# Kernel optimization log

Hardware: AMD Instinct MI355X
Metric: run time of the kernel (lower is better)

Reference implementation:

```python
import jax, jax.numpy as jnp
import numpy as np

N_NODES = 100000
F_DIM = 128      # graph.num_node_features
TE_DIM = 32      # te_emb_dim
D = F_DIM + TE_DIM  # attention embed_dim = 160
B = 4096         # number of target nodes (batched python loop)
K = 64           # candidates per target
TAU = 1.0
THRESHOLD = 0.2
EPS = 1e-10


def setup_inputs() -> dict:
    key = jax.random.key(0)
    ks = jax.random.split(key, 16)
    inp = {
        "x": jax.random.normal(ks[0], (N_NODES, F_DIM), dtype=jnp.float32),
        "target_node_ids": jax.random.randint(ks[1], (B,), 0, N_NODES),
        "target_node_times": jax.random.randint(ks[2], (B,), 1, 10000),
        "neighbor_ids": jax.random.randint(ks[3], (B, K), 0, N_NODES),
        "edge_time": jax.random.randint(ks[4], (B, K), 0, 10000),
        "edge_weight": jax.random.uniform(ks[5], (B, K), dtype=jnp.float32),
        "gumbel_u": jax.random.uniform(ks[6], (B, K), dtype=jnp.float32),
        # TemporalEncoding params: te(t) = cos(t * w + b)
        "te_w": jax.random.normal(ks[7], (TE_DIM,), dtype=jnp.float32),
        "te_b": jax.random.normal(ks[8], (TE_DIM,), dtype=jnp.float32),
        # MultiheadAttention params (packed qkv like torch)
        "in_proj_w": jax.random.normal(ks[9], (3 * D, D), dtype=jnp.float32) / np.sqrt(D),
        "in_proj_b": jnp.zeros((3 * D,), dtype=jnp.float32),
        "out_w": jax.random.normal(ks[10], (D, D), dtype=jnp.float32) / np.sqrt(D),
        "out_b": jnp.zeros((D,), dtype=jnp.float32),
        # MLP: Linear(D+1 -> 1) + LeakyReLU
        "mlp_w": jax.random.normal(ks[11], (D + 1,), dtype=jnp.float32) / np.sqrt(D + 1),
        "mlp_b": jnp.zeros((1,), dtype=jnp.float32),
    }
    return inp


def reference(x, target_node_ids, target_node_times, neighbor_ids, edge_time,
              edge_weight, gumbel_u, te_w, te_b, in_proj_w, in_proj_b,
              out_w, out_b, mlp_w, mlp_b):
    # --- build target embedding: [B, D]
    t_x = x[target_node_ids]                                          # [B, F]
    t_te = jnp.cos(target_node_times[:, None].astype(jnp.float32) * te_w + te_b)  # [B, TE]
    q_in = jnp.concatenate([t_x, t_te], axis=-1)                      # [B, D]

    # --- candidate embeddings: [B, K, D]
    c_x = x[neighbor_ids]                                             # [B, K, F]
    c_te = jnp.cos(edge_time[..., None].astype(jnp.float32) * te_w + te_b)        # [B, K, TE]
    kv_in = jnp.concatenate([c_x, c_te], axis=-1)                     # [B, K, D]

    # --- single-head MultiheadAttention (eval mode, 1 query per target)
    Wq, Wk, Wv = in_proj_w[:D], in_proj_w[D:2 * D], in_proj_w[2 * D:]
    bq, bk, bv = in_proj_b[:D], in_proj_b[D:2 * D], in_proj_b[2 * D:]
    q = q_in @ Wq.T + bq                                              # [B, D]
    k = jnp.einsum('bkf,df->bkd', kv_in, Wk) + bk                     # [B, K, D]
    v = jnp.einsum('bkf,df->bkd', kv_in, Wv) + bv                     # [B, K, D]
    scores = jnp.einsum('bd,bkd->bk', q, k) / jnp.sqrt(jnp.float32(D))
    attn_w = jax.nn.softmax(scores, axis=-1)                          # [B, K]
    ctx = jnp.einsum('bk,bkd->bd', attn_w, v)                         # [B, D]
    attn_output = ctx @ out_w.T + out_b                               # [B, D]

    # --- gumbel-softmax mask over attention weights (soft, then threshold)
    g = -jnp.log(-jnp.log(gumbel_u + EPS) + EPS)                      # gumbel(0,1)
    y_soft = jax.nn.softmax((attn_w + g) / TAU, axis=-1)
    candidate_mask = y_soft > THRESHOLD                               # [B, K] bool

    # --- MLP edge-weight update: Linear(D+1 -> 1) + LeakyReLU
    mlp_in = jnp.concatenate(
        [jnp.broadcast_to(attn_output[:, None, :], (attn_output.shape[0], edge_weight.shape[1], attn_output.shape[1])),
         edge_weight[..., None]], axis=-1)                            # [B, K, D+1]
    new_edge_weight = jax.nn.leaky_relu(jnp.einsum('bkf,f->bk', mlp_in, mlp_w) + mlp_b[0])  # [B, K]

    return attn_output, new_edge_weight, candidate_mask
```

## Files before the change

### kernel.cpp

```cpp
#include <hip/hip_runtime.h>

#define F_DIM 128
#define TE_DIM 32
#define DD 160
#define NB 4096
#define KK 64
#define ROWS 4
#define LD 164
#define TE_STRIDE 36

#define WS_M   0
#define WS_V2  25600
#define WS_C   51200
#define WS_U   51360
#define WS_B2  51520
#define WS_S0  51680
#define WS_TOT 51681

__device__ __forceinline__ float dot4acc(const float4 w, const float4 v, float a) {
    a = fmaf(w.x, v.x, a);
    a = fmaf(w.y, v.y, a);
    a = fmaf(w.z, v.z, a);
    a = fmaf(w.w, v.w, a);
    return a;
}

__device__ __forceinline__ float wave_max(float v) {
    #pragma unroll
    for (int off = 32; off > 0; off >>= 1) v = fmaxf(v, __shfl_xor(v, off, 64));
    return v;
}
__device__ __forceinline__ float wave_sum(float v) {
    #pragma unroll
    for (int off = 32; off > 0; off >>= 1) v += __shfl_xor(v, off, 64);
    return v;
}

__device__ __forceinline__ void gemv_rows(
    const float* __restrict__ W, const float* __restrict__ bias,
    const float (*vin)[LD], float (*vout)[LD], int tid)
{
    const int r  = tid & 3;
    const int dl = tid >> 2;
    const float4* v4 = (const float4*)vin[r];
    const float4* w0 = (const float4*)(W + (long)dl * DD);
    const float4* w1 = (const float4*)(W + (long)(dl + 64) * DD);
    float a0 = bias[dl];
    float a1 = bias[dl + 64];
    if (dl < 32) {
        const float4* w2 = (const float4*)(W + (long)(dl + 128) * DD);
        float a2 = bias[dl + 128];
        #pragma unroll 8
        for (int f = 0; f < 40; ++f) {
            const float4 v = v4[f];
            a0 = dot4acc(w0[f], v, a0);
            a1 = dot4acc(w1[f], v, a1);
            a2 = dot4acc(w2[f], v, a2);
        }
        vout[r][dl]       = a0;
        vout[r][dl + 64]  = a1;
        vout[r][dl + 128] = a2;
    } else {
        #pragma unroll 8
        for (int f = 0; f < 40; ++f) {
            const float4 v = v4[f];
            a0 = dot4acc(w0[f], v, a0);
            a1 = dot4acc(w1[f], v, a1);
        }
        vout[r][dl]      = a0;
        vout[r][dl + 64] = a1;
    }
}

__global__ void setup_kernel(const float* __restrict__ ipw, const float* __restrict__ ipb,
                             const float* __restrict__ ow,  const float* __restrict__ ob,
                             float* __restrict__ ws)
{
    const int g = blockIdx.x * blockDim.x + threadIdx.x;
    const float inv = 0.07905694150420949f;
    if (g < 25600) {
        const int e = g / DD, f = g % DD;
        const float* wk = ipw + DD * DD;
        float a = 0.f;
        for (int d = 0; d < DD; ++d) a = fmaf(wk[d * DD + e], ipw[d * DD + f], a);
        ws[WS_M + g] = a * inv;
    } else if (g < 51200) {
        const int gg = g - 25600;
        const int i = gg / DD, f = gg % DD;
        const float* wv = ipw + 2 * DD * DD;
        float a = 0.f;
        for (int d = 0; d < DD; ++d) a = fmaf(ow[i * DD + d], wv[d * DD + f], a);
        ws[WS_V2 + gg] = a;
    } else if (g < 51360) {
        const int e = g - 51200;
        const float* wk = ipw + DD * DD;
        float a = 0.f;
        for (int d = 0; d < DD; ++d) a = fmaf(wk[d * DD + e], ipb[d], a);
        ws[WS_C + e] = a * inv;
    } else if (g < 51520) {
        const int f = g - 51360;
        float a = 0.f;
        for (int d = 0; d < DD; ++d) a = fmaf(ipw[d * DD + f], ipb[DD + d], a);
        ws[WS_U + f] = a * inv;
    } else if (g < 51680) {
        const int i = g - 51520;
        float a = ob[i];
        for (int d = 0; d < DD; ++d) a = fmaf(ow[i * DD + d], ipb[2 * DD + d], a);
        ws[WS_B2 + i] = a;
    } else if (g == 51680) {
        float a = 0.f;
        for (int d = 0; d < DD; ++d) a = fmaf(ipb[d], ipb[DD + d], a);
        ws[WS_S0] = a * inv;
    }
}

__global__ __launch_bounds__(256, 4)
void structure_learner_kernel(
    const float* __restrict__ x,
    const int*   __restrict__ target_node_ids,
    const int*   __restrict__ target_node_times,
    const int*   __restrict__ neighbor_ids,
    const int*   __restrict__ edge_time,
    const float* __restrict__ edge_weight,
    const float* __restrict__ gumbel_u,
    const float* __restrict__ te_w,
    const float* __restrict__ te_b,
    const float* __restrict__ mlp_w,
    const float* __restrict__ mlp_b,
    const float* __restrict__ ws,
    float* __restrict__ out_ao,
    float* __restrict__ out_new,
    float* __restrict__ out_mask)
{
    __shared__ __attribute__((aligned(16))) float s_qin[ROWS][LD];
    __shared__ __attribute__((aligned(16))) float s_qt[ROWS][LD];
    __shared__ __attribute__((aligned(16))) float s_wkv[ROWS][LD];
    __shared__ __attribute__((aligned(16))) float s_ao[ROWS][LD];
    __shared__ float s_attnw[ROWS][KK];
    __shared__ int   s_nid[ROWS][KK];
    __shared__ __attribute__((aligned(4))) _Float16 s_te[ROWS][KK][TE_STRIDE];

    const int tid  = threadIdx.x;
    const int wr   = tid >> 6;
    const int lane = tid & 63;
    const int b    = blockIdx.x * ROWS + wr;

    const float* Mw = ws + WS_M;
    const float* V2 = ws + WS_V2;
    const float* Cv = ws + WS_C;
    const float* Uv = ws + WS_U;
    const float* B2 = ws + WS_B2;
    const float  s0 = ws[WS_S0];

    {
        s_nid[wr][lane] = neighbor_ids[(long)b * KK + lane];
        const float etv = (float)edge_time[(long)b * KK + lane];
        const int tn = target_node_ids[b];
        const float2 tx = *(const float2*)(x + (long)tn * F_DIM + lane * 2);
        s_qin[wr][lane * 2]     = tx.x;
        s_qin[wr][lane * 2 + 1] = tx.y;
        if (lane < TE_DIM) {
            const float tt = (float)target_node_times[b];
            s_qin[wr][F_DIM + lane] = cosf(tt * te_w[lane] + te_b[lane]);
        }
        #pragma unroll
        for (int jj = 0; jj < 16; ++jj) {
            union { _Float16 h[2]; unsigned u; } pk;
            pk.h[0] = (_Float16)cosf(etv * te_w[2 * jj]     + te_b[2 * jj]);
            pk.h[1] = (_Float16)cosf(etv * te_w[2 * jj + 1] + te_b[2 * jj + 1]);
            *(unsigned*)&s_te[wr][lane][2 * jj] = pk.u;
        }
    }
    __syncthreads();

    gemv_rows(Mw, Cv, s_qin, s_qt, tid);
    __syncthreads();

    float aw;
    {
        float p = s_qin[wr][lane] * Uv[lane];
        p = fmaf(s_qin[wr][lane + 64], Uv[lane + 64], p);
        if (lane < 32) p = fmaf(s_qin[wr][128 + lane], Uv[128 + lane], p);
        const float sbk = wave_sum(p) + s0;

        const int nidk = s_nid[wr][lane];
        const float4* xr  = (const float4*)(x + (long)nidk * F_DIM);
        const float4* qt4 = (const float4*)s_qt[wr];
        float acc = 0.f;
        #pragma unroll 8
        for (int f = 0; f < F_DIM / 4; ++f)
            acc = dot4acc(xr[f], qt4[f], acc);
        const float* qte = s_qt[wr] + F_DIM;
        #pragma unroll
        for (int jj = 0; jj < 16; ++jj) {
            union { _Float16 h[2]; unsigned u; } pk;
            pk.u = *(const unsigned*)&s_te[wr][lane][2 * jj];
            acc = fmaf(qte[2 * jj],     (float)pk.h[0], acc);
            acc = fmaf(qte[2 * jj + 1], (float)pk.h[1], acc);
        }
        const float sc = acc + sbk;
        const float m = wave_max(sc);
        const float e = expf(sc - m);
        const float l = wave_sum(e);
        aw = e / l;
        s_attnw[wr][lane] = aw;
    }

    {
        float ax = 0.f, ay = 0.f, at = 0.f;
        const float* xb = x + lane * 2;
        const int lte = lane & 31;
        #pragma unroll 8
        for (int k = 0; k < KK; ++k) {
            const float wgt = s_attnw[wr][k];
            const int   nid = s_nid[wr][k];
            const float2 xv = *(const float2*)(xb + (long)nid * F_DIM);
            ax = fmaf(wgt, xv.x, ax);
            ay = fmaf(wgt, xv.y, ay);
            at = fmaf(wgt, (float)s_te[wr][k][lte], at);
        }
        s_wkv[wr][lane * 2]     = ax;
        s_wkv[wr][lane * 2 + 1] = ay;
        if (lane < TE_DIM) s_wkv[wr][F_DIM + lane] = at;
    }
    __syncthreads();

    gemv_rows(V2, B2, s_wkv, s_ao, tid);
    __syncthreads();

    {
        float p = s_ao[wr][lane] * mlp_w[lane];
        p = fmaf(s_ao[wr][lane + 64], mlp_w[lane + 64], p);
        if (lane < 32) p = fmaf(s_ao[wr][lane + 128], mlp_w[lane + 128], p);
        const float base = wave_sum(p) + mlp_b[0];

        float* ao = out_ao + (long)b * DD;
        ao[lane]      = s_ao[wr][lane];
        ao[lane + 64] = s_ao[wr][lane + 64];
        if (lane < 32) ao[lane + 128] = s_ao[wr][lane + 128];

        const float u = gumbel_u[(long)b * KK + lane];
        const float g = -logf(-logf(u + 1e-10f) + 1e-10f);
        const float z = aw + g;
        const float m = wave_max(z);
        const float e = expf(z - m);
        const float l = wave_sum(e);
        out_mask[(long)b * KK + lane] = (e / l > 0.2f) ? 1.0f : 0.0f;

        const float ew  = edge_weight[(long)b * KK + lane];
        const float val = fmaf(ew, mlp_w[DD], base);
        out_new[(long)b * KK + lane] = (val >= 0.f) ? val : 0.01f * val;
    }
}

extern "C" void kernel_launch(void* const* d_in, const int* in_sizes, int n_in,
                              void* d_out, int out_size, void* d_ws, size_t ws_size,
                              hipStream_t stream) {
    const float* x   = (const float*)d_in[0];
    const int*   tni = (const int*)d_in[1];
    const int*   tnt = (const int*)d_in[2];
    const int*   nid = (const int*)d_in[3];
    const int*   et  = (const int*)d_in[4];
    const float* ew  = (const float*)d_in[5];
    const float* gu  = (const float*)d_in[6];
    const float* tew = (const float*)d_in[7];
    const float* teb = (const float*)d_in[8];
    const float* ipw = (const float*)d_in[9];
    const float* ipb = (const float*)d_in[10];
    const float* ow  = (const float*)d_in[11];
    const float* ob  = (const float*)d_in[12];
    const float* mw  = (const float*)d_in[13];
    const float* mb  = (const float*)d_in[14];

    float* wsf = (float*)d_ws;

    float* out      = (float*)d_out;
    float* out_ao   = out;
    float* out_new  = out + (long)NB * DD;
    float* out_mask = out + (long)NB * DD + (long)NB * KK;

    setup_kernel<<<(WS_TOT + 255) / 256, 256, 0, stream>>>(ipw, ipb, ow, ob, wsf);

    structure_learner_kernel<<<NB / ROWS, 256, 0, stream>>>(
        x, tni, tnt, nid, et, ew, gu, tew, teb, mw, mb, wsf,
        out_ao, out_new, out_mask);
}
```

Measured before the change: 178.5 us.

## Split fused kernel into batched q-projection, attention, and output-projection kernels

Splits the single per-row kernel into three kernels. The two 160x160 GEMVs now run as small batched GEMMs over 16 rows per block, so each weight load is reused across 16 rows instead of 4. The score computation is reorganised so each half-wave reads a contiguous float4 slice of a neighbor row and reduces with shuffles, giving coalesced gathers instead of one lane walking a whole row. The cost is extra global round-trips through the workspace for q-projections, score bias and weighted values, plus two more kernel launches.

```diff
diff --git a/kernel.cpp b/kernel.cpp
--- a/kernel.cpp
+++ b/kernel.cpp
@@ -5,17 +5,17 @@
 #define DD 160
 #define NB 4096
 #define KK 64
-#define ROWS 4
-#define LD 164
-#define TE_STRIDE 36
-
-#define WS_M   0
-#define WS_V2  25600
-#define WS_C   51200
-#define WS_U   51360
-#define WS_B2  51520
-#define WS_S0  51680
-#define WS_TOT 51681
+
+#define WS_M    0
+#define WS_V2   25600
+#define WS_C    51200
+#define WS_U    51360
+#define WS_B2   51520
+#define WS_S0   51680
+#define WS_WTOT 51681
+#define WS_QT   51712
+#define WS_SBK  707072
+#define WS_WKV  711168
 
 __device__ __forceinline__ float dot4acc(const float4 w, const float4 v, float a) {
     a = fmaf(w.x, v.x, a);
@@ -24,7 +24,6 @@
     a = fmaf(w.w, v.w, a);
     return a;
 }
-
 __device__ __forceinline__ float wave_max(float v) {
     #pragma unroll
     for (int off = 32; off > 0; off >>= 1) v = fmaxf(v, __shfl_xor(v, off, 64));
@@ -34,42 +33,6 @@
     #pragma unroll
     for (int off = 32; off > 0; off >>= 1) v += __shfl_xor(v, off, 64);
     return v;
-}
-
-__device__ __forceinline__ void gemv_rows(
-    const float* __restrict__ W, const float* __restrict__ bias,
-    const float (*vin)[LD], float (*vout)[LD], int tid)
-{
-    const int r  = tid & 3;
-    const int dl = tid >> 2;
-    const float4* v4 = (const float4*)vin[r];
-    const float4* w0 = (const float4*)(W + (long)dl * DD);
-    const float4* w1 = (const float4*)(W + (long)(dl + 64) * DD);
-    float a0 = bias[dl];
-    float a1 = bias[dl + 64];
-    if (dl < 32) {
-        const float4* w2 = (const float4*)(W + (long)(dl + 128) * DD);
-        float a2 = bias[dl + 128];
-        #pragma unroll 8
-        for (int f = 0; f < 40; ++f) {
-            const float4 v = v4[f];
-            a0 = dot4acc(w0[f], v, a0);
-            a1 = dot4acc(w1[f], v, a1);
-            a2 = dot4acc(w2[f], v, a2);
-        }
-        vout[r][dl]       = a0;
-        vout[r][dl + 64]  = a1;
-        vout[r][dl + 128] = a2;
-    } else {
-        #pragma unroll 8
-        for (int f = 0; f < 40; ++f) {
-            const float4 v = v4[f];
-            a0 = dot4acc(w0[f], v, a0);
-            a1 = dot4acc(w1[f], v, a1);
-        }
-        vout[r][dl]      = a0;
-        vout[r][dl + 64] = a1;
-    }
 }
 
 __global__ void setup_kernel(const float* __restrict__ ipw, const float* __restrict__ ipb,
@@ -114,55 +77,88 @@
     }
 }
 
+__global__ __launch_bounds__(256)
+void qt_kernel(const float* __restrict__ x,
+               const int* __restrict__ tni, const int* __restrict__ tnt,
+               const float* __restrict__ te_w, const float* __restrict__ te_b,
+               float* __restrict__ ws)
+{
+    __shared__ __attribute__((aligned(16))) float s_qin[16][164];
+    __shared__ int   s_tn[16];
+    __shared__ float s_tt[16];
+    const int t  = threadIdx.x;
+    const int b0 = blockIdx.x * 16;
+
+    if (t < 16) { s_tn[t] = tni[b0 + t]; s_tt[t] = (float)tnt[b0 + t]; }
+    __syncthreads();
+
+    {
+        const int r = t >> 4, seg = t & 15;
+        const float4* src = (const float4*)(x + (long)s_tn[r] * F_DIM + seg * 8);
+        const float4 a = src[0], bq = src[1];
+        *(float4*)&s_qin[r][seg * 8]     = a;
+        *(float4*)&s_qin[r][seg * 8 + 4] = bq;
+        const int j2 = seg * 2;
+        s_qin[r][F_DIM + j2]     = cosf(s_tt[r] * te_w[j2]     + te_b[j2]);
+        s_qin[r][F_DIM + j2 + 1] = cosf(s_tt[r] * te_w[j2 + 1] + te_b[j2 + 1]);
+    }
+    __syncthreads();
+
+    {
+        const int r = t >> 4, seg = t & 15;
+        const float* U = ws + WS_U;
+        float p = 0.f;
+        #pragma unroll
+        for (int i = 0; i < 10; ++i) p = fmaf(s_qin[r][seg * 10 + i], U[seg * 10 + i], p);
+        #pragma unroll
+        for (int off = 1; off < 16; off <<= 1) p += __shfl_xor(p, off, 64);
+        if (seg == 0) ws[WS_SBK + b0 + r] = p + ws[WS_S0];
+    }
+
+    {
+        const int r = t & 15, eg = t >> 4;
+        const float* M = ws + WS_M;
+        const float* C = ws + WS_C;
+        float acc[10];
+        #pragma unroll
+        for (int j = 0; j < 10; ++j) acc[j] = C[eg * 10 + j];
+        for (int f0 = 0; f0 < DD; f0 += 8) {
+            const float4 q0 = *(const float4*)&s_qin[r][f0];
+            const float4 q1 = *(const float4*)&s_qin[r][f0 + 4];
+            #pragma unroll
+            for (int j = 0; j < 10; ++j) {
+                const float4* mp = (const float4*)(M + (long)(eg * 10 + j) * DD + f0);
+                acc[j] = dot4acc(mp[0], q0, acc[j]);
+                acc[j] = dot4acc(mp[1], q1, acc[j]);
+            }
+        }
+        float* qt = ws + WS_QT + (long)(b0 + r) * DD + eg * 10;
+        #pragma unroll
+        for (int j = 0; j < 10; ++j) qt[j] = acc[j];
+    }
+}
+
 __global__ __launch_bounds__(256, 4)
-void structure_learner_kernel(
-    const float* __restrict__ x,
-    const int*   __restrict__ target_node_ids,
-    const int*   __restrict__ target_node_times,
-    const int*   __restrict__ neighbor_ids,
-    const int*   __restrict__ edge_time,
-    const float* __restrict__ edge_weight,
-    const float* __restrict__ gumbel_u,
-    const float* __restrict__ te_w,
-    const float* __restrict__ te_b,
-    const float* __restrict__ mlp_w,
-    const float* __restrict__ mlp_b,
-    const float* __restrict__ ws,
-    float* __restrict__ out_ao,
-    float* __restrict__ out_new,
-    float* __restrict__ out_mask)
+void attn_kernel(const float* __restrict__ x,
+                 const int* __restrict__ neighbor_ids,
+                 const int* __restrict__ edge_time,
+                 const float* __restrict__ gumbel_u,
+                 const float* __restrict__ te_w, const float* __restrict__ te_b,
+                 float* __restrict__ ws,
+                 float* __restrict__ out_mask)
 {
-    __shared__ __attribute__((aligned(16))) float s_qin[ROWS][LD];
-    __shared__ __attribute__((aligned(16))) float s_qt[ROWS][LD];
-    __shared__ __attribute__((aligned(16))) float s_wkv[ROWS][LD];
-    __shared__ __attribute__((aligned(16))) float s_ao[ROWS][LD];
-    __shared__ float s_attnw[ROWS][KK];
-    __shared__ int   s_nid[ROWS][KK];
-    __shared__ __attribute__((aligned(4))) _Float16 s_te[ROWS][KK][TE_STRIDE];
-
-    const int tid  = threadIdx.x;
-    const int wr   = tid >> 6;
-    const int lane = tid & 63;
-    const int b    = blockIdx.x * ROWS + wr;
-
-    const float* Mw = ws + WS_M;
-    const float* V2 = ws + WS_V2;
-    const float* Cv = ws + WS_C;
-    const float* Uv = ws + WS_U;
-    const float* B2 = ws + WS_B2;
-    const float  s0 = ws[WS_S0];
-
-    {
-        s_nid[wr][lane] = neighbor_ids[(long)b * KK + lane];
-        const float etv = (float)edge_time[(long)b * KK + lane];
-        const int tn = target_node_ids[b];
-        const float2 tx = *(const float2*)(x + (long)tn * F_DIM + lane * 2);
-        s_qin[wr][lane * 2]     = tx.x;
-        s_qin[wr][lane * 2 + 1] = tx.y;
-        if (lane < TE_DIM) {
-            const float tt = (float)target_node_times[b];
-            s_qin[wr][F_DIM + lane] = cosf(tt * te_w[lane] + te_b[lane]);
-        }
+    __shared__ __attribute__((aligned(4))) _Float16 s_te[4][KK][36];
+    __shared__ int   s_nid[4][KK];
+    __shared__ float s_sc[4][KK];
+    __shared__ float s_aw[4][KK];
+    __shared__ float s_qte[4][TE_DIM];
+
+    const int tid = threadIdx.x, wr = tid >> 6, lane = tid & 63;
+    const long b = (long)blockIdx.x * 4 + wr;
+
+    {
+        s_nid[wr][lane] = neighbor_ids[b * KK + lane];
+        const float etv = (float)edge_time[b * KK + lane];
         #pragma unroll
         for (int jj = 0; jj < 16; ++jj) {
             union { _Float16 h[2]; unsigned u; } pk;
@@ -171,39 +167,53 @@
             *(unsigned*)&s_te[wr][lane][2 * jj] = pk.u;
         }
     }
-    __syncthreads();
-
-    gemv_rows(Mw, Cv, s_qin, s_qt, tid);
-    __syncthreads();
+    const int fl = lane & 31, half = lane >> 5;
+    const float4 qf = *(const float4*)(ws + WS_QT + b * DD + 4 * fl);
+    if (lane < TE_DIM) s_qte[wr][lane] = ws[WS_QT + b * DD + F_DIM + lane];
+    const float sbk = ws[WS_SBK + b];
+
+    float tedot = 0.f;
+    #pragma unroll
+    for (int jj = 0; jj < 16; ++jj) {
+        union { _Float16 h[2]; unsigned u; } pk;
+        pk.u = *(const unsigned*)&s_te[wr][lane][2 * jj];
+        tedot = fmaf(s_qte[wr][2 * jj],     (float)pk.h[0], tedot);
+        tedot = fmaf(s_qte[wr][2 * jj + 1], (float)pk.h[1], tedot);
+    }
+
+    #pragma unroll 4
+    for (int i = 0; i < 32; ++i) {
+        const int k  = 2 * i + half;
+        const int nk = s_nid[wr][k];
+        const float4 xv = *(const float4*)(x + (long)nk * F_DIM + 4 * fl);
+        float p = 0.f;
+        p = dot4acc(xv, qf, p);
+        p += __shfl_xor(p, 16, 64);
+        p += __shfl_xor(p, 8, 64);
+        p += __shfl_xor(p, 4, 64);
+        p += __shfl_xor(p, 2, 64);
+        p += __shfl_xor(p, 1, 64);
+        if (fl == 0) s_sc[wr][k] = p;
+    }
 
     float aw;
     {
-        float p = s_qin[wr][lane] * Uv[lane];
-        p = fmaf(s_qin[wr][lane + 64], Uv[lane + 64], p);
-        if (lane < 32) p = fmaf(s_qin[wr][128 + lane], Uv[128 + lane], p);
-        const float sbk = wave_sum(p) + s0;
-
-        const int nidk = s_nid[wr][lane];
-        const float4* xr  = (const float4*)(x + (long)nidk * F_DIM);
-        const float4* qt4 = (const float4*)s_qt[wr];
-        float acc = 0.f;
-        #pragma unroll 8
-        for (int f = 0; f < F_DIM / 4; ++f)
-            acc = dot4acc(xr[f], qt4[f], acc);
-        const float* qte = s_qt[wr] + F_DIM;
-        #pragma unroll
-        for (int jj = 0; jj < 16; ++jj) {
-            union { _Float16 h[2]; unsigned u; } pk;
-            pk.u = *(const unsigned*)&s_te[wr][lane][2 * jj];
-            acc = fmaf(qte[2 * jj],     (float)pk.h[0], acc);
-            acc = fmaf(qte[2 * jj + 1], (float)pk.h[1], acc);
-        }
-        const float sc = acc + sbk;
+        const float sc = s_sc[wr][lane] + tedot + sbk;
         const float m = wave_max(sc);
         const float e = expf(sc - m);
         const float l = wave_sum(e);
         aw = e / l;
-        s_attnw[wr][lane] = aw;
+        s_aw[wr][lane] = aw;
+    }
+
+    {
+        const float u = gumbel_u[b * KK + lane];
+        const float g = -logf(-logf(u + 1e-10f) + 1e-10f);
+        const float z = aw + g;
+        const float m = wave_max(z);
+        const float e = expf(z - m);
+        const float l = wave_sum(e);
+        out_mask[b * KK + lane] = (e / l > 0.2f) ? 1.0f : 0.0f;
     }
 
     {
@@ -212,44 +222,84 @@
         const int lte = lane & 31;
         #pragma unroll 8
         for (int k = 0; k < KK; ++k) {
-            const float wgt = s_attnw[wr][k];
-            const int   nid = s_nid[wr][k];
-            const float2 xv = *(const float2*)(xb + (long)nid * F_DIM);
+            const float wgt = s_aw[wr][k];
+            const int   nk  = s_nid[wr][k];
+            const float2 xv = *(const float2*)(xb + (long)nk * F_DIM);
             ax = fmaf(wgt, xv.x, ax);
             ay = fmaf(wgt, xv.y, ay);
             at = fmaf(wgt, (float)s_te[wr][k][lte], at);
         }
-        s_wkv[wr][lane * 2]     = ax;
-        s_wkv[wr][lane * 2 + 1] = ay;
-        if (lane < TE_DIM) s_wkv[wr][F_DIM + lane] = at;
-    }
-    __syncthreads();
-
-    gemv_rows(V2, B2, s_wkv, s_ao, tid);
-    __syncthreads();
-
-    {
-        float p = s_ao[wr][lane] * mlp_w[lane];
-        p = fmaf(s_ao[wr][lane + 64], mlp_w[lane + 64], p);
-        if (lane < 32) p = fmaf(s_ao[wr][lane + 128], mlp_w[lane + 128], p);
-        const float base = wave_sum(p) + mlp_b[0];
-
-        float* ao = out_ao + (long)b * DD;
-        ao[lane]      = s_ao[wr][lane];
-        ao[lane + 64] = s_ao[wr][lane + 64];
-        if (lane < 32) ao[lane + 128] = s_ao[wr][lane + 128];
-
-        const float u = gumbel_u[(long)b * KK + lane];
-        const float g = -logf(-logf(u + 1e-10f) + 1e-10f);
-        const float z = aw + g;
-        const float m = wave_max(z);
-        const float e = expf(z - m);
-        const float l = wave_sum(e);
-        out_mask[(long)b * KK + lane] = (e / l > 0.2f) ? 1.0f : 0.0f;
-
-        const float ew  = edge_weight[(long)b * KK + lane];
-        const float val = fmaf(ew, mlp_w[DD], base);
-        out_new[(long)b * KK + lane] = (val >= 0.f) ? val : 0.01f * val;
+        float* wkv = ws + WS_WKV + b * DD;
+        wkv[lane * 2]     = ax;
+        wkv[lane * 2 + 1] = ay;
+        if (lane < TE_DIM) wkv[F_DIM + lane] = at;
+    }
+}
+
+__global__ __launch_bounds__(256)
+void ao_kernel(const float* __restrict__ edge_weight,
+               const float* __restrict__ mlp_w, const float* __restrict__ mlp_b,
+               float* __restrict__ ws,
+               float* __restrict__ out_ao, float* __restrict__ out_new)
+{
+    __shared__ __attribute__((aligned(16))) float s_v[16][164];
+    __shared__ __attribute__((aligned(16))) float s_ao[16][164];
+    __shared__ float s_base[16];
+    const int t  = threadIdx.x;
+    const int b0 = blockIdx.x * 16;
+
+    #pragma unroll
+    for (int c = 0; c < 10; ++c) {
+        const int idx = t + 256 * c;
+        s_v[idx / DD][idx % DD] = ws[WS_WKV + (long)b0 * DD + idx];
+    }
+    __syncthreads();
+
+    {
+        const int r = t & 15, eg = t >> 4;
+        const float* V2 = ws + WS_V2;
+        const float* B2 = ws + WS_B2;
+        float acc[10];
+        #pragma unroll
+        for (int j = 0; j < 10; ++j) acc[j] = B2[eg * 10 + j];
+        for (int f0 = 0; f0 < DD; f0 += 8) {
+            const float4 q0 = *(const float4*)&s_v[r][f0];
+            const float4 q1 = *(const float4*)&s_v[r][f0 + 4];
+            #pragma unroll
+            for (int j = 0; j < 10; ++j) {
+                const float4* mp = (const float4*)(V2 + (long)(eg * 10 + j) * DD + f0);
+                acc[j] = dot4acc(mp[0], q0, acc[j]);
+                acc[j] = dot4acc(mp[1], q1, acc[j]);
+            }
+        }
+        #pragma unroll
+        for (int j = 0; j < 10; ++j) s_ao[r][eg * 10 + j] = acc[j];
+    }
+    __syncthreads();
+
+    {
+        const int r = t >> 4, seg = t & 15;
+        float p = 0.f;
+        #pragma unroll
+        for (int i = 0; i < 10; ++i) p = fmaf(s_ao[r][seg * 10 + i], mlp_w[seg * 10 + i], p);
+        #pragma unroll
+        for (int off = 1; off < 16; off <<= 1) p += __shfl_xor(p, off, 64);
+        if (seg == 0) s_base[r] = p + mlp_b[0];
+    }
+    __syncthreads();
+
+    #pragma unroll
+    for (int c = 0; c < 10; ++c) {
+        const int idx = t + 256 * c;
+        out_ao[(long)b0 * DD + idx] = s_ao[idx / DD][idx % DD];
+    }
+    #pragma unroll
+    for (int c = 0; c < 4; ++c) {
+        const int idx = t + 256 * c;
+        const int r = idx >> 6, kx = idx & 63;
+        const float ew  = edge_weight[(long)(b0 + r) * KK + kx];
+        const float val = fmaf(ew, mlp_w[DD], s_base[r]);
+        out_new[(long)(b0 + r) * KK + kx] = (val >= 0.f) ? val : 0.01f * val;
     }
 }
 
@@ -279,9 +329,8 @@
     float* out_new  = out + (long)NB * DD;
     float* out_mask = out + (long)NB * DD + (long)NB * KK;
 
-    setup_kernel<<<(WS_TOT + 255) / 256, 256, 0, stream>>>(ipw, ipb, ow, ob, wsf);
-
-    structure_learner_kernel<<<NB / ROWS, 256, 0, stream>>>(
-        x, tni, tnt, nid, et, ew, gu, tew, teb, mw, mb, wsf,
-        out_ao, out_new, out_mask);
-}
+    setup_kernel<<<(WS_WTOT + 255) / 256, 256, 0, stream>>>(ipw, ipb, ow, ob, wsf);
+    qt_kernel<<<NB / 16, 256, 0, stream>>>(x, tni, tnt, tew, teb, wsf);
+    attn_kernel<<<NB / 4, 256, 0, stream>>>(x, nid, et, gu, tew, teb, wsf, out_mask);
+    ao_kernel<<<NB / 16, 256, 0, stream>>>(ew, mw, mb, wsf, out_ao, out_new);
+}
```

Measured after the change: 195.1 us. 1.09x slower.
